# Kernel optimization log

Measured on AMD Instinct MI355X. Metric: run time of the kernel, lower is better.

The kernel has to match this reference:

```python
import jax, jax.numpy as jnp
import numpy as np

B = 4096
D_IN = 1024
H1 = 2048
H2 = 1024
E = 7          # num_experts, forced by broadcasting in source
T = 2          # num_tasks
NS = 7         # scene dimension of S
EMB_ROWS = 10
EMB_DIM = 16


def setup_inputs() -> dict:
    key = jax.random.key(0)
    ks = jax.random.split(key, 8)
    x = jax.random.normal(ks[0], (B, D_IN), dtype=jnp.float32)
    scene = jax.random.randint(ks[1], (B,), 0, E)
    # Expert MLP params, stacked over experts: Linear(D_IN->H1)+ReLU, Linear(H1->H2)+ReLU
    W1 = jax.random.normal(ks[2], (E, D_IN, H1), dtype=jnp.float32) * (1.0 / np.sqrt(D_IN))
    b1 = jnp.zeros((E, H1), dtype=jnp.float32)
    W2 = jax.random.normal(ks[3], (E, H1, H2), dtype=jnp.float32) * (1.0 / np.sqrt(H1))
    b2 = jnp.zeros((E, H2), dtype=jnp.float32)
    # Routing tensor S: [7, input_dim+16, num_experts] (xavier-like init)
    S = jax.random.normal(ks[4], (NS, D_IN + EMB_DIM, E), dtype=jnp.float32) * 0.02
    scene_emb = jax.random.normal(ks[5], (EMB_ROWS, EMB_DIM), dtype=jnp.float32)
    return {"x": x, "scene": scene, "W1": W1, "b1": b1, "W2": W2, "b2": b2,
            "S": S, "scene_emb": scene_emb}


def _forward(x, scene, W1, b1, W2, b2, S, scene_emb):
    # Experts (vectorized over the E expert MLPs): [B,E,H2]
    h = jax.nn.relu(jnp.einsum('bd,edh->beh', x, W1) + b1)
    experts_out = jax.nn.relu(jnp.einsum('beh,eho->beo', h, W2) + b2)

    se = scene_emb[scene]                       # [B,16]
    xc = jnp.concatenate([x, se], axis=-1)      # [B, D_IN+16]
    G = jnp.einsum('bd,sde->bse', xc, S)        # [B, 7, E]
    G = jnp.transpose(G, (0, 2, 1))             # [B, E, 7]
    G = jax.nn.softmax(G, axis=-1)

    logG = jnp.log(G)                           # [B, E, 7]
    q = jnp.sum(jnp.log(G * 7.0) / 7.0, axis=-1)  # [B, E]

    KG = jnp.eye(E, dtype=x.dtype)
    ses = KG[scene][:, None, :]                 # [B, 1, E]

    _, pi = jax.lax.top_k(jnp.sum(ses * logG, axis=-1), 6)  # [B,6]
    _, qi = jax.lax.top_k(q, 6)                              # [B,6]
    select = ((KG[pi].sum(axis=1) + KG[qi].sum(axis=1)) > 0).astype(x.dtype)  # [B,E]

    gate = jax.nn.softmax(jnp.sum(G * ses, axis=-1), axis=-1) * select  # [B,E]
    out = jnp.einsum('be,bed->bd', gate, experts_out)                    # [B,H2]
    # self.gate ModuleList is unused in the source forward; each task output is identical
    return jnp.stack([out] * T, axis=0)         # [T, B, H2]


def reference(x, scene, W1, b1, W2, b2, S, scene_emb):
    return _forward(x, scene, W1, b1, W2, b2, S, scene_emb)
```

## Files before the change

kernel.cpp:

```cpp
#include <hip/hip_runtime.h>
#include <hip/hip_bf16.h>

typedef unsigned short u16;
typedef __bf16 bf8 __attribute__((ext_vector_type(8)));
typedef float f4 __attribute__((ext_vector_type(4)));

__device__ __forceinline__ u16 f2bf(float f) {
    unsigned int u = __float_as_uint(f);
    u = (u + 0x7fffu + ((u >> 16) & 1u)) >> 16;
    return (u16)u;
}

__device__ __forceinline__ void gload16(const u16* g, u16* l) {
    __builtin_amdgcn_global_load_lds((const __attribute__((address_space(1))) void*)g,
                                     (__attribute__((address_space(3))) void*)l, 16, 0, 0);
}

__global__ void cvt_x_kernel(const float* __restrict__ in, u16* __restrict__ out, int n4) {
    int i = blockIdx.x * blockDim.x + threadIdx.x;
    int stride = gridDim.x * blockDim.x;
    for (; i < n4; i += stride) {
        float4 v = ((const float4*)in)[i];
        ushort4 o;
        o.x = f2bf(v.x); o.y = f2bf(v.y); o.z = f2bf(v.z); o.w = f2bf(v.w);
        ((ushort4*)out)[i] = o;
    }
}

__global__ void transpose_cvt_kernel(const float* __restrict__ in, u16* __restrict__ out,
                                     int R, int C) {
    __shared__ float t[32][33];
    int e = blockIdx.z;
    int c0 = blockIdx.x * 32, r0 = blockIdx.y * 32;
    int tx = threadIdx.x & 31, ty = threadIdx.x >> 5;
    const float* ip = in + (size_t)e * R * C;
    u16* op = out + (size_t)e * R * C;
#pragma unroll
    for (int k = 0; k < 32; k += 8)
        t[ty + k][tx] = ip[(size_t)(r0 + ty + k) * C + c0 + tx];
    __syncthreads();
#pragma unroll
    for (int k = 0; k < 32; k += 8)
        op[(size_t)(c0 + ty + k) * R + r0 + tx] = f2bf(t[tx][ty + k]);
}

__global__ void transpose_S_kernel(const float* __restrict__ S, float* __restrict__ ST) {
    int idx = blockIdx.x * 256 + threadIdx.x;
    if (idx >= 1040 * 52) return;
    int d = idx / 52, c = idx % 52;
    ST[idx] = (c < 49) ? S[(c / 7) * 7280 + d * 7 + (c % 7)] : 0.f;
}

__global__ void gating_kernel(const float* __restrict__ x, const int* __restrict__ scene,
                              const float* __restrict__ ST, const float* __restrict__ semb,
                              float* __restrict__ gate) {
    __shared__ float xc[4][1040];
    __shared__ float Lsh[4][49];
    int wv = threadIdx.x >> 6, lane = threadIdx.x & 63;
    int row = blockIdx.x * 4 + wv;
    float* xcw = xc[wv];
    const float* xr = x + (size_t)row * 1024;
    for (int d = lane; d < 1024; d += 64) xcw[d] = xr[d];
    int sc = scene[row];
    if (lane < 16) xcw[1024 + lane] = semb[sc * 16 + lane];
    __syncthreads();

    if (lane < 49) {
        const float* STp = ST + lane;
        float a0 = 0.f, a1 = 0.f, a2 = 0.f, a3 = 0.f;
        for (int d = 0; d < 1040; d += 4) {
            a0 += xcw[d]     * STp[d * 52];
            a1 += xcw[d + 1] * STp[d * 52 + 52];
            a2 += xcw[d + 2] * STp[d * 52 + 104];
            a3 += xcw[d + 3] * STp[d * 52 + 156];
        }
        Lsh[wv][lane] = (a0 + a1) + (a2 + a3);
    }
    __syncthreads();

    if (lane == 0) {
        float logG[7][7], Gsc[7], piS[7], qS[7];
        for (int e = 0; e < 7; e++) {
            float L[7];
            float m = -1e30f;
            for (int s = 0; s < 7; s++) { L[s] = Lsh[wv][s * 7 + e]; m = fmaxf(m, L[s]); }
            float sum = 0.f;
            for (int s = 0; s < 7; s++) sum += expf(L[s] - m);
            float lse = m + logf(sum);
            float qs = 0.f;
            for (int s = 0; s < 7; s++) { logG[e][s] = L[s] - lse; qs += logG[e][s]; }
            piS[e] = logG[e][sc];
            qS[e] = qs;
            Gsc[e] = expf(logG[e][sc]);
        }
        int epi = 0, eqi = 0; float bp = piS[0], bq = qS[0];
        for (int e = 1; e < 7; e++) {
            if (piS[e] <= bp) { bp = piS[e]; epi = e; }
            if (qS[e]  <= bq) { bq = qS[e];  eqi = e; }
        }
        float mg = -1e30f;
        for (int e = 0; e < 7; e++) mg = fmaxf(mg, Gsc[e]);
        float sum = 0.f;
        float ex[7];
        for (int e = 0; e < 7; e++) { ex[e] = expf(Gsc[e] - mg); sum += ex[e]; }
        float inv = 1.f / sum;
        for (int e = 0; e < 7; e++) {
            float g = ex[e] * inv;
            if (e == epi && e == eqi) g = 0.f;
            gate[row * 7 + e] = g;
        }
    }
}

template<bool G2>
__global__ __launch_bounds__(512, 2) void gemmE_kernel(
    const u16* __restrict__ Abase, const u16* __restrict__ Bbase,
    const float* __restrict__ bias, const float* __restrict__ gate,
    void* __restrict__ outp)
{
    constexpr int M = 4096;
    constexpr int K = G2 ? 2048 : 1024;
    constexpr int N = G2 ? 1024 : 2048;
    constexpr int NT = K / 64;
    constexpr int BNT = N / 256;

    extern __shared__ u16 lds[];

    const int tid = threadIdx.x;
    const int lane = tid & 63;
    const int wid = tid >> 6;
    const int wr = wid >> 2, wc = wid & 3;
    const int ln15 = lane & 15, lnk = (lane >> 4) * 8;

    const int nwg = gridDim.x, cpx = nwg >> 3;
    const int wg = (blockIdx.x & 7) * cpx + (blockIdx.x >> 3);
    const int e  = wg / (16 * BNT);
    const int rem = wg % (16 * BNT);
    const int bm = rem / BNT, bn = rem % BNT;

    const u16* Ae = Abase + (G2 ? (size_t)e * M * K : (size_t)0);
    const u16* Be = Bbase + (size_t)e * N * K;

    const int sr = tid >> 3;
    const int sc = (tid & 7) * 8;

    auto stageA = [&](int kt, int buf) {
#pragma unroll
        for (int l = 0; l < 4; ++l) {
            int r = l * 64 + sr;
            int cs = sc ^ ((r & 7) << 3);
            const u16* g = Ae + (size_t)(bm * 256 + r) * K + kt * 64 + cs;
            gload16(g, lds + buf * 32768 + l * 4096 + tid * 8);
        }
    };
    auto stageB = [&](int kt, int buf, int h) {
#pragma unroll
        for (int l = 0; l < 2; ++l) {
            int rb = h * 128 + l * 64 + sr;
            int cs = sc ^ ((rb & 7) << 3);
            const u16* g = Be + (size_t)(bn * 256 + rb) * K + kt * 64 + cs;
            gload16(g, lds + buf * 32768 + 16384 + h * 8192 + l * 4096 + tid * 8);
        }
    };
    auto aoff = [&](int mi, int ks) {
        int r = wr * 128 + mi * 16 + ln15;
        int c = ks * 32 + lnk;
        return r * 64 + (c ^ ((r & 7) << 3));
    };
    auto boff = [&](int ni, int ks) {
        int rb = wc * 64 + ni * 16 + ln15;
        int c = ks * 32 + lnk;
        return rb * 64 + (c ^ ((rb & 7) << 3));
    };

    f4 acc[8][4] = {};
    bf8 aA[4][2], bL[2][2], bH[2][2];

    stageA(0, 0); stageB(0, 0, 0); stageB(0, 0, 1);

    for (int gt = 0; gt < NT; ++gt) {
        const int cur = gt & 1, nxt = cur ^ 1;
        const bool more = (gt + 1 < NT);
        const u16* Ac = lds + cur * 32768;
        const u16* Bc = lds + cur * 32768 + 16384;
        if (more) {
            stageA(gt + 1, nxt);
            asm volatile("s_waitcnt vmcnt(4)" ::: "memory");
        } else {
            asm volatile("s_waitcnt vmcnt(0)" ::: "memory");
        }
        __builtin_amdgcn_sched_barrier(0);
        __builtin_amdgcn_s_barrier();
        __builtin_amdgcn_sched_barrier(0);
#pragma unroll
        for (int mi = 0; mi < 4; ++mi)
#pragma unroll
            for (int ks = 0; ks < 2; ++ks)
                aA[mi][ks] = *(const bf8*)(Ac + aoff(mi, ks));
#pragma unroll
        for (int ni = 0; ni < 2; ++ni)
#pragma unroll
            for (int ks = 0; ks < 2; ++ks)
                bL[ni][ks] = *(const bf8*)(Bc + boff(ni, ks));
        asm volatile("s_waitcnt lgkmcnt(0)" ::: "memory");
        __builtin_amdgcn_sched_barrier(0);
        __builtin_amdgcn_s_setprio(1);
#pragma unroll
        for (int mi = 0; mi < 4; ++mi)
#pragma unroll
            for (int ni = 0; ni < 2; ++ni)
#pragma unroll
                for (int ks = 0; ks < 2; ++ks)
                    acc[mi][ni] = __builtin_amdgcn_mfma_f32_16x16x32_bf16(aA[mi][ks], bL[ni][ks], acc[mi][ni], 0, 0, 0);
        __builtin_amdgcn_s_setprio(0);
        if (more) stageB(gt + 1, nxt, 0);
#pragma unroll
        for (int ni = 0; ni < 2; ++ni)
#pragma unroll
            for (int ks = 0; ks < 2; ++ks)
                bH[ni][ks] = *(const bf8*)(Bc + boff(2 + ni, ks));
        asm volatile("s_waitcnt lgkmcnt(0)" ::: "memory");
        __builtin_amdgcn_sched_barrier(0);
        __builtin_amdgcn_s_setprio(1);
#pragma unroll
        for (int mi = 0; mi < 4; ++mi)
#pragma unroll
            for (int ni = 0; ni < 2; ++ni)
#pragma unroll
                for (int ks = 0; ks < 2; ++ks)
                    acc[mi][2 + ni] = __builtin_amdgcn_mfma_f32_16x16x32_bf16(aA[mi][ks], bH[ni][ks], acc[mi][2 + ni], 0, 0, 0);
        __builtin_amdgcn_s_setprio(0);
        if (more) stageB(gt + 1, nxt, 1);
#pragma unroll
        for (int mi = 0; mi < 4; ++mi)
#pragma unroll
            for (int ks = 0; ks < 2; ++ks)
                aA[mi][ks] = *(const bf8*)(Ac + aoff(4 + mi, ks));
        asm volatile("s_waitcnt lgkmcnt(0)" ::: "memory");
        __builtin_amdgcn_sched_barrier(0);
        __builtin_amdgcn_s_setprio(1);
#pragma unroll
        for (int mi = 0; mi < 4; ++mi)
#pragma unroll
            for (int ni = 0; ni < 2; ++ni)
#pragma unroll
                for (int ks = 0; ks < 2; ++ks)
                    acc[4 + mi][2 + ni] = __builtin_amdgcn_mfma_f32_16x16x32_bf16(aA[mi][ks], bH[ni][ks], acc[4 + mi][2 + ni], 0, 0, 0);
        __builtin_amdgcn_s_setprio(0);
        __builtin_amdgcn_sched_barrier(0);
        __builtin_amdgcn_s_barrier();
        __builtin_amdgcn_sched_barrier(0);
        __builtin_amdgcn_s_setprio(1);
#pragma unroll
        for (int mi = 0; mi < 4; ++mi)
#pragma unroll
            for (int ni = 0; ni < 2; ++ni)
#pragma unroll
                for (int ks = 0; ks < 2; ++ks)
                    acc[4 + mi][ni] = __builtin_amdgcn_mfma_f32_16x16x32_bf16(aA[mi][ks], bL[ni][ks], acc[4 + mi][ni], 0, 0, 0);
        __builtin_amdgcn_s_setprio(0);
        __builtin_amdgcn_sched_barrier(0);
    }

    float bloc[4];
#pragma unroll
    for (int ni = 0; ni < 4; ++ni)
        bloc[ni] = bias[e * N + bn * 256 + wc * 64 + ni * 16 + ln15];
    if constexpr (G2) {
        float* part = (float*)outp;
#pragma unroll
        for (int mi = 0; mi < 8; ++mi)
#pragma unroll
            for (int i = 0; i < 4; ++i) {
                int row = bm * 256 + wr * 128 + mi * 16 + (lane >> 4) * 4 + i;
                float g = gate[row * 7 + e];
#pragma unroll
                for (int ni = 0; ni < 4; ++ni) {
                    float v = g * fmaxf(acc[mi][ni][i] + bloc[ni], 0.f);
                    atomicAdd(&part[(size_t)row * N + bn * 256 + wc * 64 + ni * 16 + ln15], v);
                }
            }
    } else {
        u16* Hp = (u16*)outp + (size_t)e * M * N;
#pragma unroll
        for (int mi = 0; mi < 8; ++mi)
#pragma unroll
            for (int i = 0; i < 4; ++i) {
                size_t row = (size_t)(bm * 256 + wr * 128 + mi * 16 + (lane >> 4) * 4 + i);
#pragma unroll
                for (int ni = 0; ni < 4; ++ni)
                    Hp[row * N + bn * 256 + wc * 64 + ni * 16 + ln15] =
                        f2bf(fmaxf(acc[mi][ni][i] + bloc[ni], 0.f));
            }
    }
}

__global__ void combine_kernel(const float* __restrict__ part, float* __restrict__ out, int n4) {
    int i = blockIdx.x * blockDim.x + threadIdx.x;
    int stride = gridDim.x * blockDim.x;
    for (; i < n4; i += stride) {
        float4 v = ((const float4*)part)[i];
        ((float4*)out)[i] = v;
        ((float4*)out)[i + n4] = v;
    }
}

extern "C" void kernel_launch(void* const* d_in, const int* in_sizes, int n_in,
                              void* d_out, int out_size, void* d_ws, size_t ws_size,
                              hipStream_t stream) {
    const float* x     = (const float*)d_in[0];
    const int*   scene = (const int*)d_in[1];
    const float* W1    = (const float*)d_in[2];
    const float* b1    = (const float*)d_in[3];
    const float* W2    = (const float*)d_in[4];
    const float* b2    = (const float*)d_in[5];
    const float* S     = (const float*)d_in[6];
    const float* semb  = (const float*)d_in[7];
    float* out = (float*)d_out;

    char* ws = (char*)d_ws;
    float* part = (float*)(ws);
    u16*   xb   = (u16*)(ws);
    u16*   W1T  = (u16*)(ws + 8388608);
    u16*   W2T  = (u16*)(ws + 37748736);
    u16*   Hb   = (u16*)(ws + 67108864);
    float* gate = (float*)(ws + 184549376);
    float* ST   = (float*)(ws + 184664064);

    (void)hipFuncSetAttribute(reinterpret_cast<const void*>(gemmE_kernel<false>),
                              hipFuncAttributeMaxDynamicSharedMemorySize, 131072);
    (void)hipFuncSetAttribute(reinterpret_cast<const void*>(gemmE_kernel<true>),
                              hipFuncAttributeMaxDynamicSharedMemorySize, 131072);

    cvt_x_kernel<<<2048, 256, 0, stream>>>(x, xb, 4096 * 1024 / 4);
    transpose_cvt_kernel<<<dim3(64, 32, 7), 256, 0, stream>>>(W1, W1T, 1024, 2048);
    transpose_cvt_kernel<<<dim3(32, 64, 7), 256, 0, stream>>>(W2, W2T, 2048, 1024);
    transpose_S_kernel<<<(1040 * 52 + 255) / 256, 256, 0, stream>>>(S, ST);
    gating_kernel<<<1024, 256, 0, stream>>>(x, scene, ST, semb, gate);
    gemmE_kernel<false><<<896, 512, 131072, stream>>>(xb, W1T, b1, nullptr, Hb);
    (void)hipMemsetAsync(part, 0, (size_t)4096 * 1024 * 4, stream);
    gemmE_kernel<true><<<448, 512, 131072, stream>>>(Hb, W2T, b2, gate, part);
    combine_kernel<<<2048, 256, 0, stream>>>(part, out, 4096 * 1024 / 4);
}
```

Measured before the change: 423.3 us.

## Issue all next-tile loads upfront and split LDS reads with partial lgkmcnt waits

Moves the global-to-LDS staging of the next A and both B halves to the top of each K iteration, waiting with vmcnt(8) instead of interleaving the B stages mid-iteration. LDS fragment reads are split into halves with partial lgkmcnt waits, so MFMA work on the first half can start while the second half is still in flight. The goal is to hide LDS read latency and give global loads a longer window. In exchange, more memory traffic is in flight at the barrier, and the vmcnt count must match the number of loads each staging call issues.

```diff
diff --git a/kernel.cpp b/kernel.cpp
--- a/kernel.cpp
+++ b/kernel.cpp
@@ -183,9 +183,10 @@
         const bool more = (gt + 1 < NT);
         const u16* Ac = lds + cur * 32768;
         const u16* Bc = lds + cur * 32768 + 16384;
+
         if (more) {
-            stageA(gt + 1, nxt);
-            asm volatile("s_waitcnt vmcnt(4)" ::: "memory");
+            stageA(gt + 1, nxt); stageB(gt + 1, nxt, 0); stageB(gt + 1, nxt, 1);
+            asm volatile("s_waitcnt vmcnt(8)" ::: "memory");
         } else {
             asm volatile("s_waitcnt vmcnt(0)" ::: "memory");
         }
@@ -193,60 +194,104 @@
         __builtin_amdgcn_s_barrier();
         __builtin_amdgcn_sched_barrier(0);
 #pragma unroll
+        for (int ni = 0; ni < 2; ++ni)
+#pragma unroll
+            for (int ks = 0; ks < 2; ++ks)
+                bL[ni][ks] = *(const bf8*)(Bc + boff(ni, ks));
+#pragma unroll
+        for (int mi = 0; mi < 2; ++mi)
+#pragma unroll
+            for (int ks = 0; ks < 2; ++ks)
+                aA[mi][ks] = *(const bf8*)(Ac + aoff(mi, ks));
+        __builtin_amdgcn_sched_barrier(0);
+#pragma unroll
+        for (int mi = 2; mi < 4; ++mi)
+#pragma unroll
+            for (int ks = 0; ks < 2; ++ks)
+                aA[mi][ks] = *(const bf8*)(Ac + aoff(mi, ks));
+        asm volatile("s_waitcnt lgkmcnt(4)" ::: "memory");
+        __builtin_amdgcn_sched_barrier(0);
+        __builtin_amdgcn_s_setprio(1);
+#pragma unroll
+        for (int mi = 0; mi < 2; ++mi)
+#pragma unroll
+            for (int ni = 0; ni < 2; ++ni)
+#pragma unroll
+                for (int ks = 0; ks < 2; ++ks)
+                    acc[mi][ni] = __builtin_amdgcn_mfma_f32_16x16x32_bf16(aA[mi][ks], bL[ni][ks], acc[mi][ni], 0, 0, 0);
+        __builtin_amdgcn_s_setprio(0);
+        asm volatile("s_waitcnt lgkmcnt(0)" ::: "memory");
+        __builtin_amdgcn_sched_barrier(0);
+        __builtin_amdgcn_s_setprio(1);
+#pragma unroll
+        for (int mi = 2; mi < 4; ++mi)
+#pragma unroll
+            for (int ni = 0; ni < 2; ++ni)
+#pragma unroll
+                for (int ks = 0; ks < 2; ++ks)
+                    acc[mi][ni] = __builtin_amdgcn_mfma_f32_16x16x32_bf16(aA[mi][ks], bL[ni][ks], acc[mi][ni], 0, 0, 0);
+        __builtin_amdgcn_s_setprio(0);
+
+#pragma unroll
+        for (int ks = 0; ks < 2; ++ks)
+            bH[0][ks] = *(const bf8*)(Bc + boff(2, ks));
+        __builtin_amdgcn_sched_barrier(0);
+#pragma unroll
+        for (int ks = 0; ks < 2; ++ks)
+            bH[1][ks] = *(const bf8*)(Bc + boff(3, ks));
+        asm volatile("s_waitcnt lgkmcnt(2)" ::: "memory");
+        __builtin_amdgcn_sched_barrier(0);
+        __builtin_amdgcn_s_setprio(1);
+#pragma unroll
         for (int mi = 0; mi < 4; ++mi)
 #pragma unroll
             for (int ks = 0; ks < 2; ++ks)
-                aA[mi][ks] = *(const bf8*)(Ac + aoff(mi, ks));
-#pragma unroll
-        for (int ni = 0; ni < 2; ++ni)
-#pragma unroll
-            for (int ks = 0; ks < 2; ++ks)
-                bL[ni][ks] = *(const bf8*)(Bc + boff(ni, ks));
+                acc[mi][2] = __builtin_amdgcn_mfma_f32_16x16x32_bf16(aA[mi][ks], bH[0][ks], acc[mi][2], 0, 0, 0);
+        __builtin_amdgcn_s_setprio(0);
         asm volatile("s_waitcnt lgkmcnt(0)" ::: "memory");
         __builtin_amdgcn_sched_barrier(0);
         __builtin_amdgcn_s_setprio(1);
 #pragma unroll
         for (int mi = 0; mi < 4; ++mi)
 #pragma unroll
-            for (int ni = 0; ni < 2; ++ni)
-#pragma unroll
-                for (int ks = 0; ks < 2; ++ks)
-                    acc[mi][ni] = __builtin_amdgcn_mfma_f32_16x16x32_bf16(aA[mi][ks], bL[ni][ks], acc[mi][ni], 0, 0, 0);
-        __builtin_amdgcn_s_setprio(0);
-        if (more) stageB(gt + 1, nxt, 0);
-#pragma unroll
-        for (int ni = 0; ni < 2; ++ni)
-#pragma unroll
-            for (int ks = 0; ks < 2; ++ks)
-                bH[ni][ks] = *(const bf8*)(Bc + boff(2 + ni, ks));
+            for (int ks = 0; ks < 2; ++ks)
+                acc[mi][3] = __builtin_amdgcn_mfma_f32_16x16x32_bf16(aA[mi][ks], bH[1][ks], acc[mi][3], 0, 0, 0);
+        __builtin_amdgcn_s_setprio(0);
+
+#pragma unroll
+        for (int mi = 0; mi < 2; ++mi)
+#pragma unroll
+            for (int ks = 0; ks < 2; ++ks)
+                aA[mi][ks] = *(const bf8*)(Ac + aoff(4 + mi, ks));
+        __builtin_amdgcn_sched_barrier(0);
+#pragma unroll
+        for (int mi = 2; mi < 4; ++mi)
+#pragma unroll
+            for (int ks = 0; ks < 2; ++ks)
+                aA[mi][ks] = *(const bf8*)(Ac + aoff(4 + mi, ks));
+        asm volatile("s_waitcnt lgkmcnt(4)" ::: "memory");
+        __builtin_amdgcn_sched_barrier(0);
+        __builtin_amdgcn_s_setprio(1);
+#pragma unroll
+        for (int mi = 0; mi < 2; ++mi)
+#pragma unroll
+            for (int ni = 2; ni < 4; ++ni)
+#pragma unroll
+                for (int ks = 0; ks < 2; ++ks)
+                    acc[4 + mi][ni] = __builtin_amdgcn_mfma_f32_16x16x32_bf16(aA[mi][ks], bH[ni - 2][ks], acc[4 + mi][ni], 0, 0, 0);
+        __builtin_amdgcn_s_setprio(0);
         asm volatile("s_waitcnt lgkmcnt(0)" ::: "memory");
         __builtin_amdgcn_sched_barrier(0);
         __builtin_amdgcn_s_setprio(1);
 #pragma unroll
-        for (int mi = 0; mi < 4; ++mi)
-#pragma unroll
-            for (int ni = 0; ni < 2; ++ni)
-#pragma unroll
-                for (int ks = 0; ks < 2; ++ks)
-                    acc[mi][2 + ni] = __builtin_amdgcn_mfma_f32_16x16x32_bf16(aA[mi][ks], bH[ni][ks], acc[mi][2 + ni], 0, 0, 0);
-        __builtin_amdgcn_s_setprio(0);
-        if (more) stageB(gt + 1, nxt, 1);
-#pragma unroll
-        for (int mi = 0; mi < 4; ++mi)
-#pragma unroll
-            for (int ks = 0; ks < 2; ++ks)
-                aA[mi][ks] = *(const bf8*)(Ac + aoff(4 + mi, ks));
-        asm volatile("s_waitcnt lgkmcnt(0)" ::: "memory");
-        __builtin_amdgcn_sched_barrier(0);
-        __builtin_amdgcn_s_setprio(1);
-#pragma unroll
-        for (int mi = 0; mi < 4; ++mi)
-#pragma unroll
-            for (int ni = 0; ni < 2; ++ni)
-#pragma unroll
-                for (int ks = 0; ks < 2; ++ks)
-                    acc[4 + mi][2 + ni] = __builtin_amdgcn_mfma_f32_16x16x32_bf16(aA[mi][ks], bH[ni][ks], acc[4 + mi][2 + ni], 0, 0, 0);
-        __builtin_amdgcn_s_setprio(0);
+        for (int mi = 2; mi < 4; ++mi)
+#pragma unroll
+            for (int ni = 2; ni < 4; ++ni)
+#pragma unroll
+                for (int ks = 0; ks < 2; ++ks)
+                    acc[4 + mi][ni] = __builtin_amdgcn_mfma_f32_16x16x32_bf16(aA[mi][ks], bH[ni - 2][ks], acc[4 + mi][ni], 0, 0, 0);
+        __builtin_amdgcn_s_setprio(0);
+
         __builtin_amdgcn_sched_barrier(0);
         __builtin_amdgcn_s_barrier();
         __builtin_amdgcn_sched_barrier(0);
```

Result: slower. 432.0 us (+2.1%).
